# Kernel tuning notes

Hardware: AMD Instinct MI355X
Metric: run time of the kernel (lower is better)

## Reference

```python
import jax, jax.numpy as jnp
import numpy as np

ENERGY = 0.4  # target low-frequency energy ratio (ctor default energy=0.4)


def setup_inputs() -> dict:
    key = jax.random.key(0)
    x = jax.random.normal(key, (8, 64, 256, 256), dtype=jnp.float32)
    return {"x": x}


def _min_cutoff_map(H, W):
    """For each pixel of the fftshifted spectrum, the smallest cutoff c such that
    the pixel lies inside the central box [crow-c:crow+c, ccol-c:ccol+c].
    A pixel (r, cc) is inside iff c >= max(-dr, dr+1) and c >= max(-dc, dc+1)."""
    crow, ccol = H // 2, W // 2
    dr = np.arange(H) - crow
    dc = np.arange(W) - ccol
    mr = np.maximum(-dr, dr + 1)
    mc = np.maximum(-dc, dc + 1)
    return np.maximum(mr[:, None], mc[None, :]).astype(np.int32)  # [H, W]


def reference(x):
    B, C, H, W = x.shape
    # fp32 FFT (matches the autocast-disabled fft in the original)
    fshift = jnp.fft.fftshift(jnp.fft.fft2(x.astype(jnp.float32)), axes=(-2, -1))

    minc = jnp.asarray(_min_cutoff_map(H, W))          # [H, W] int32
    nseg = max(H // 2, W // 2) + 1                      # static
    K = min(H, W) // 2                                  # candidates are 1..K-1

    # Radial (box) cumulative energy profile of channel 0, one pass per sample.
    mag2 = jnp.abs(fshift[:, 0]) ** 2                   # [B, H, W]
    ids = minc.reshape(-1)
    per_box = jax.vmap(
        lambda m: jax.ops.segment_sum(m.reshape(-1), ids, num_segments=nseg)
    )(mag2)                                             # [B, nseg]
    cum = jnp.cumsum(per_box, axis=-1)                  # cum[b, c] = box-energy at cutoff c
    total = cum[:, -1]
    target = ENERGY * total

    found = cum[:, 1:K] >= target[:, None]              # candidates c = 1..K-1
    first = jnp.argmax(found, axis=-1) + 1              # smallest satisfying c
    cutoff = jnp.where(jnp.any(found, axis=-1), first, 5)  # fallback 5, as in torch

    # Zero the central box per sample (broadcast over channels), then inverse FFT.
    keep = (minc[None, None, :, :] > cutoff[:, None, None, None]).astype(jnp.float32)
    hp = fshift * keep
    out = jnp.abs(jnp.fft.ifft2(jnp.fft.ifftshift(hp, axes=(-2, -1))))
    return out
```

## Files before the change

### kernel.cpp

```cpp
#include <hip/hip_runtime.h>
#include <hip/hip_fp16.h>
#include <math.h>

#define RESERVE 16384

__device__ __forceinline__ float2 cadd(float2 a, float2 b){ return make_float2(a.x+b.x, a.y+b.y); }
__device__ __forceinline__ float2 csub(float2 a, float2 b){ return make_float2(a.x-b.x, a.y-b.y); }
__device__ __forceinline__ float2 cmul(float2 a, float2 b){ return make_float2(a.x*b.x - a.y*b.y, a.x*b.y + a.y*b.x); }
__device__ __forceinline__ float2 cmulc(float2 a, float2 b){
  return make_float2(a.x*b.x + a.y*b.y, a.x*b.y - a.y*b.x); }
__device__ __forceinline__ __half2 f2h(float2 v){ return __floats2half2_rn(v.x, v.y); }
__device__ __forceinline__ float2 h2f(__half2 h){ return __half22float2(h); }

#define SCHED_FENCE() __builtin_amdgcn_sched_barrier(0x7F)

__device__ __forceinline__ constexpr int rho4(int r) { return ((r & 3) << 2) | (r >> 2); }

template<int DIR> __device__ __forceinline__ float2 twc(float2 z, float c, float s) {
  const float si = (DIR < 0) ? s : -s;
  return make_float2(c*z.x - si*z.y, c*z.y + si*z.x);
}
template<int DIR> __device__ __forceinline__ float2 mulmi(float2 z) {
  return (DIR < 0) ? make_float2(z.y, -z.x) : make_float2(-z.y, z.x);
}

template<int DIR, bool REV>
__device__ __forceinline__ void fft16(float2* v) {
  #define IX(i) (REV ? rho4(i) : (i))
  #pragma unroll
  for (int j0 = 0; j0 < 4; ++j0) {
    float2 a0 = v[IX(j0)], a1 = v[IX(j0+4)], a2 = v[IX(j0+8)], a3 = v[IX(j0+12)];
    float2 t0 = cadd(a0,a2), t1 = csub(a0,a2), t2 = cadd(a1,a3), d = csub(a1,a3);
    float2 t3 = (DIR < 0) ? make_float2(d.y,-d.x) : make_float2(-d.y,d.x);
    v[IX(j0)]    = cadd(t0,t2);
    v[IX(j0+4)]  = cadd(t1,t3);
    v[IX(j0+8)]  = csub(t0,t2);
    v[IX(j0+12)] = csub(t1,t3);
  }
  v[IX(5)]  = twc<DIR>(v[IX(5)],  0.92387953f, -0.38268343f);
  v[IX(6)]  = twc<DIR>(v[IX(6)],  0.70710678f, -0.70710678f);
  v[IX(7)]  = twc<DIR>(v[IX(7)],  0.38268343f, -0.92387953f);
  v[IX(9)]  = twc<DIR>(v[IX(9)],  0.70710678f, -0.70710678f);
  v[IX(10)] = mulmi<DIR>(v[IX(10)]);
  v[IX(11)] = twc<DIR>(v[IX(11)], -0.70710678f, -0.70710678f);
  v[IX(13)] = twc<DIR>(v[IX(13)],  0.38268343f, -0.92387953f);
  v[IX(14)] = twc<DIR>(v[IX(14)], -0.70710678f, -0.70710678f);
  v[IX(15)] = twc<DIR>(v[IX(15)], -0.92387953f,  0.38268343f);
  #pragma unroll
  for (int k1 = 0; k1 < 4; ++k1) {
    float2 a0 = v[IX(4*k1)], a1 = v[IX(4*k1+1)], a2 = v[IX(4*k1+2)], a3 = v[IX(4*k1+3)];
    float2 t0 = cadd(a0,a2), t1 = csub(a0,a2), t2 = cadd(a1,a3), d = csub(a1,a3);
    float2 t3 = (DIR < 0) ? make_float2(d.y,-d.x) : make_float2(-d.y,d.x);
    v[IX(4*k1)]   = cadd(t0,t2);
    v[IX(4*k1+1)] = cadd(t1,t3);
    v[IX(4*k1+2)] = csub(t0,t2);
    v[IX(4*k1+3)] = csub(t1,t3);
  }
  #undef IX
}

__device__ __forceinline__ void make_twf(int l, float2* twf) {
  float s, c;
  sincospif((float)l * (-1.0f/128.0f), &s, &c);
  const float2 w = make_float2(c, s);
  twf[0] = make_float2(1.f, 0.f);
  #pragma unroll
  for (int k = 1; k < 16; ++k) twf[k] = cmul(twf[k-1], w);
}

template<int DIR, bool REV1, bool HB>
__device__ __forceinline__ void fft256g(float2* v, void* trb, int l, const float2* twf) {
  fft16<DIR, REV1>(v);
  if (HB) {
    __half2* t = (__half2*)trb;
    #pragma unroll
    for (int r = 0; r < 16; ++r) {
      const int k1 = REV1 ? r : rho4(r);
      float2 z = v[r];
      z = (DIR < 0) ? cmul(twf[k1], z) : cmulc(twf[k1], z);
      t[k1 * 17 + l] = f2h(z);
    }
    SCHED_FENCE();
    #pragma unroll
    for (int j = 0; j < 16; ++j) v[j] = h2f(t[l * 17 + j]);
  } else {
    float2* t = (float2*)trb;
    #pragma unroll
    for (int r = 0; r < 16; ++r) {
      const int k1 = REV1 ? r : rho4(r);
      float2 z = v[r];
      z = (DIR < 0) ? cmul(twf[k1], z) : cmulc(twf[k1], z);
      t[k1 * 17 + l] = z;
    }
    SCHED_FENCE();
    #pragma unroll
    for (int j = 0; j < 16; ++j) v[j] = ((float2*)trb)[l * 17 + j];
  }
  SCHED_FENCE();
  fft16<DIR, false>(v);
}

#define GS32 276
#define GS16 280

__device__ __forceinline__ int SW(int row, int col) {
  return (row << 8) + (col ^ ((row & 7) << 2) ^ ((row & 1) << 4));
}
__device__ __forceinline__ int SW16(int r, int ul) {
  return (r << 4) + (ul ^ (r & 14));
}


__global__ __launch_bounds__(256) void k_pass1(const float* __restrict__ x,
    __half2* __restrict__ Bt, int img0, int istep) {
  __shared__ __align__(16) char smraw[16384];
  __shared__ __align__(16) float2 trbf[16 * GS32];
  float*   rowstage = (float*)smraw;
  __half2* outtile  = (__half2*)smraw;
  const int tid = threadIdx.x, g = tid >> 4, l = tid & 15;
  const int slot = blockIdx.y, img = img0 + slot * istep;
  const int r0 = blockIdx.x << 4;
  float2 twf[16]; make_twf(l, twf);
  const float* xsrc = x + ((size_t)img << 16) + (r0 << 8);
  #pragma unroll
  for (int it = 0; it < 4; ++it) {
    const int L = it * 1024 + tid * 4;
    const float4 d = *reinterpret_cast<const float4*>(xsrc + L);
    *reinterpret_cast<float4*>(rowstage + SW(L >> 8, L & 255)) = d;
  }
  __syncthreads();
  float2 v[16];
  #pragma unroll
  for (int j = 0; j < 16; ++j)
    v[j] = make_float2(rowstage[SW(g, l + (j << 4))], 0.f);
  __syncthreads();
  fft256g<-1, false, false>(v, trbf + g * GS32, l, twf);
  #pragma unroll
  for (int rr = 0; rr < 16; ++rr)
    outtile[SW(g, l + (rho4(rr) << 4))] = f2h(v[rr]);
  __syncthreads();
  __half2* bdst = Bt + ((size_t)slot << 16) + (r0 << 4);
  #pragma unroll
  for (int it = 0; it < 4; ++it) {
    const int L = it * 1024 + tid * 4;
    const int p = L >> 8, rl = (L >> 4) & 15, ul0 = L & 15;
    const int4 d = *reinterpret_cast<const int4*>(outtile + SW(rl, (p << 4) + ul0));
    *reinterpret_cast<int4*>(bdst + (p << 12) + (L & 255)) = d;
  }
}

__global__ __launch_bounds__(256) void k_pass2(const __half2* __restrict__ Bt,
    __half2* __restrict__ Ct, const int* __restrict__ cutoffs, int img0, int istep) {
  __shared__ __align__(16) char smraw[16384];
  __shared__ __align__(16) __half2 trbh[16 * GS16];
  __half2* instage = (__half2*)smraw;
  __half2* outtile = (__half2*)smraw;
  const int tid = threadIdx.x, g = tid >> 4, l = tid & 15;
  const int slot = blockIdx.y, img = img0 + slot * istep;
  const int p = blockIdx.x;
  const int cut = cutoffs[img >> 6];
  const __half2* bsrc = Bt + ((size_t)slot << 16) + (p << 12);
  __half2* cdst = Ct + ((size_t)slot << 16) + (p << 12);
  const bool kept = (p * 16 >= cut) && (p * 16 + 15 < 256 - cut);
  if (kept) {
    const __half2 s = __floats2half2_rn(256.f, 256.f);
    #pragma unroll
    for (int it = 0; it < 4; ++it) {
      const int L = it * 1024 + tid * 4;
      int4 d = *reinterpret_cast<const int4*>(bsrc + L);
      __half2* h = reinterpret_cast<__half2*>(&d);
      h[0] = __hmul2(h[0], s); h[1] = __hmul2(h[1], s);
      h[2] = __hmul2(h[2], s); h[3] = __hmul2(h[3], s);
      *reinterpret_cast<int4*>(cdst + L) = d;
    }
    return;
  }
  float2 twf[16]; make_twf(l, twf);
  #pragma unroll
  for (int it = 0; it < 4; ++it) {
    const int L = it * 1024 + tid * 4;
    const int4 d = *reinterpret_cast<const int4*>(bsrc + L);
    const int r = L >> 4, ul0 = L & 15;
    const int i0 = SW16(r, ul0);
    *reinterpret_cast<int2*>(instage + i0) = make_int2(d.x, d.y);
    *reinterpret_cast<int2*>(instage + (i0 ^ 2)) = make_int2(d.z, d.w);
  }
  __syncthreads();
  __half2 hv[16];
  #pragma unroll
  for (int j = 0; j < 16; ++j) hv[j] = instage[SW16(l + (j << 4), g)];
  __syncthreads();
  const int u = (p << 4) + g;
  float2 v[16];
  #pragma unroll
  for (int j = 0; j < 16; ++j) v[j] = h2f(hv[j]);
  fft256g<-1, false, true>(v, trbh + g * GS16, l, twf);
  if ((u < cut) | (u >= 256 - cut)) {
    #pragma unroll
    for (int rr = 0; rr < 16; ++rr) {
      const int vi = l + (rho4(rr) << 4);
      if (vi < cut || vi >= 256 - cut) v[rr] = make_float2(0.f, 0.f);
    }
  }
  fft256g<1, true, true>(v, trbh + g * GS16, l, twf);
  #pragma unroll
  for (int rr = 0; rr < 16; ++rr)
    outtile[SW16(l + (rho4(rr) << 4), g)] = f2h(v[rr]);
  __syncthreads();
  #pragma unroll
  for (int it = 0; it < 4; ++it) {
    const int L = it * 1024 + tid * 4;
    const int r = L >> 4, ul0 = L & 15;
    const int i0 = SW16(r, ul0);
    const int2 a = *reinterpret_cast<const int2*>(outtile + i0);
    const int2 b = *reinterpret_cast<const int2*>(outtile + (i0 ^ 2));
    *reinterpret_cast<int4*>(cdst + L) = make_int4(a.x, a.y, b.x, b.y);
  }
}

__global__ __launch_bounds__(256) void k_pass3(const __half2* __restrict__ Ct,
    float* __restrict__ out, int img0, int istep) {
  __shared__ __align__(16) char smraw[16384];
  __shared__ __align__(16) __half2 trbh[16 * GS16];
  __half2* instage  = (__half2*)smraw;
  float*   outstage = (float*)smraw;
  const int tid = threadIdx.x, g = tid >> 4, l = tid & 15;
  const int slot = blockIdx.y, img = img0 + slot * istep;
  const int r0 = blockIdx.x << 4;
  float2 twf[16]; make_twf(l, twf);
  #pragma unroll
  for (int k = 0; k < 16; ++k) { twf[k].x *= 0.0625f; twf[k].y *= 0.0625f; }
  const __half2* csrc = Ct + ((size_t)slot << 16) + (r0 << 4);
  #pragma unroll
  for (int it = 0; it < 4; ++it) {
    const int L = it * 1024 + tid * 4;
    const int p = L >> 8, rl = (L >> 4) & 15, ul0 = L & 15;
    const int4 d = *reinterpret_cast<const int4*>(csrc + (p << 12) + (L & 255));
    *reinterpret_cast<int4*>(instage + SW(rl, (p << 4) + ul0)) = d;
  }
  __syncthreads();
  __half2 hv[16];
  #pragma unroll
  for (int j = 0; j < 16; ++j) hv[j] = instage[SW(g, l + (j << 4))];
  __syncthreads();
  float2 v[16];
  #pragma unroll
  for (int j = 0; j < 16; ++j) v[j] = h2f(hv[j]);
  fft256g<1, false, true>(v, trbh + g * GS16, l, twf);
  #pragma unroll
  for (int rr = 0; rr < 16; ++rr) {
    const float2 z = v[rr];
    outstage[SW(g, l + (rho4(rr) << 4))] =
        __builtin_amdgcn_sqrtf(z.x*z.x + z.y*z.y) * (1.f/4096.f);
  }
  __syncthreads();
  float* odst = out + ((size_t)img << 16) + (r0 << 8);
  #pragma unroll
  for (int it = 0; it < 4; ++it) {
    const int L = it * 1024 + tid * 4;
    const float4 d = *reinterpret_cast<const float4*>(outstage + SW(L >> 8, L & 255));
    *reinterpret_cast<float4*>(odst + L) = d;
  }
}

__global__ __launch_bounds__(256) void k_hist(const __half2* __restrict__ Bt,
    double* __restrict__ bins, int slot0, int sstep, int batch0) {
  __shared__ __align__(16) __half2 instage[4096];
  __shared__ __align__(16) float2 trbf[16 * GS32];
  __shared__ float whist[4][132];
  const int tid = threadIdx.x, g = tid >> 4, l = tid & 15, wave = tid >> 6;
  const int lb = blockIdx.y;
  const int batch = batch0 + lb;
  const size_t slot = (size_t)(slot0 + lb * sstep);
  const int p = blockIdx.x;
  const int u = (p << 4) + g;
  float2 twf[16]; make_twf(l, twf);
  for (int i = tid & 63; i < 132; i += 64) whist[wave][i] = 0.f;
  const __half2* bsrc = Bt + (slot << 16) + (p << 12);
  #pragma unroll
  for (int it = 0; it < 4; ++it) {
    const int L = it * 1024 + tid * 4;
    const int4 d = *reinterpret_cast<const int4*>(bsrc + L);
    const int r = L >> 4, ul0 = L & 15;
    const int i0 = SW16(r, ul0);
    *reinterpret_cast<int2*>(instage + i0) = make_int2(d.x, d.y);
    *reinterpret_cast<int2*>(instage + (i0 ^ 2)) = make_int2(d.z, d.w);
  }
  __syncthreads();
  float2 v[16];
  #pragma unroll
  for (int j = 0; j < 16; ++j) v[j] = h2f(instage[SW16(l + (j << 4), g)]);
  fft256g<-1, false, false>(v, trbf + g * GS32, l, twf);
  const int fc = (u < 128) ? u + 1 : 256 - u;
  #pragma unroll
  for (int rr = 0; rr < 16; ++rr) {
    const int vi = l + (rho4(rr) << 4);
    const int fu = (vi < 128) ? vi + 1 : 256 - vi;
    const int seg = fu > fc ? fu : fc;
    const float2 z = v[rr];
    atomicAdd(&whist[wave][seg], z.x*z.x + z.y*z.y);
  }
  __syncthreads();
  for (int s = tid; s < 129; s += 256) {
    const float sum = whist[0][s] + whist[1][s] + whist[2][s] + whist[3][s];
    if (sum != 0.f) atomicAdd(&bins[batch * 129 + s], (double)sum);
  }
}

__global__ void k_cutoff(const double* __restrict__ bins, int* __restrict__ cutoffs) {
  const int b = threadIdx.x;
  if (b < 8) {
    const double* Bv = bins + b * 129;
    double total = 0.0;
    for (int s = 0; s < 129; ++s) total += Bv[s];
    const double target = 0.4 * total;
    double cum = Bv[0];
    int cut = 5;
    bool found = false;
    for (int s = 1; s <= 127; ++s) {
      cum += Bv[s];
      if (!found && cum >= target) { cut = s; found = true; }
    }
    cutoffs[b] = cut;
  }
}

extern "C" void kernel_launch(void* const* d_in, const int* in_sizes, int n_in,
                              void* d_out, int out_size, void* d_ws, size_t ws_size,
                              hipStream_t stream) {
  const float* x = (const float*)d_in[0];
  float* out = (float*)d_out;
  char* wsb = (char*)d_ws;
  double* bins    = (double*)wsb;
  int*    cutoffs = (int*)(wsb + 8448);
  char*   payload = wsb + RESERVE;

  size_t avail = (ws_size > RESERVE) ? ws_size - (size_t)RESERVE : 0;
  long long Gl = (long long)(avail / 524288);
  int G = (Gl > 512) ? 512 : (int)Gl;
  if (G < 1) G = 1;
  __half2* Bt = (__half2*)payload;
  __half2* Ct = (__half2*)(payload + (size_t)G * 262144);

  hipMemsetAsync(bins, 0, 8 * 129 * sizeof(double), stream);
  dim3 blk(256, 1, 1);

  if (G >= 512) {
    k_pass1<<<dim3(16, 512), blk, 0, stream>>>(x, Bt, 0, 1);
    k_hist <<<dim3(16, 8),   blk, 0, stream>>>(Bt, bins, 0, 64, 0);
    k_cutoff<<<dim3(1), dim3(64), 0, stream>>>(bins, cutoffs);
    k_pass2<<<dim3(16, 512), blk, 0, stream>>>(Bt, Ct, cutoffs, 0, 1);
    k_pass3<<<dim3(16, 512), blk, 0, stream>>>(Ct, out, 0, 1);
  } else {
    int Gp = G > 8 ? 8 : G;
    for (int b0 = 0; b0 < 8; b0 += Gp) {
      int n = (8 - b0 < Gp) ? (8 - b0) : Gp;
      k_pass1<<<dim3(16, n), blk, 0, stream>>>(x, Bt, b0 * 64, 64);
      k_hist <<<dim3(16, n), blk, 0, stream>>>(Bt, bins, 0, 1, b0);
    }
    k_cutoff<<<dim3(1), dim3(64), 0, stream>>>(bins, cutoffs);
    for (int g0 = 0; g0 < 512; g0 += G) {
      int n = (512 - g0 < G) ? (512 - g0) : G;
      k_pass1<<<dim3(16, n), blk, 0, stream>>>(x, Bt, g0, 1);
      k_pass2<<<dim3(16, n), blk, 0, stream>>>(Bt, Ct, cutoffs, g0, 1);
      k_pass3<<<dim3(16, n), blk, 0, stream>>>(Ct, out, g0, 1);
    }
  }
}
```

Measured before the change: 207.8 us.

## Exploit real-input Hermitian symmetry and alias shared-memory staging buffers

Pass1 now writes only column panels 0..8 of the row-FFT output for non-channel-0 images, since the input is real and the remaining columns are conjugates. Pass2 rebuilds the upper column panels by reading the mirrored column and negating its imaginary part. The separate transpose scratch buffers are merged into the staging buffer to cut LDS per block, which needs extra barriers. In exchange it adds strided uncoalesced column gathers in pass2, and channel 0 still writes all panels for the histogram.

Measured after the change: 216.8 us. +4.3%, slower.

```diff
diff --git a/kernel.cpp b/kernel.cpp
--- a/kernel.cpp
+++ b/kernel.cpp
@@ -113,13 +113,14 @@
 
 __global__ __launch_bounds__(256) void k_pass1(const float* __restrict__ x,
     __half2* __restrict__ Bt, int img0, int istep) {
-  __shared__ __align__(16) char smraw[16384];
-  __shared__ __align__(16) float2 trbf[16 * GS32];
+  __shared__ __align__(16) char smraw[16 * GS32 * 8];
   float*   rowstage = (float*)smraw;
   __half2* outtile  = (__half2*)smraw;
+  float2*  trbf     = (float2*)smraw;
   const int tid = threadIdx.x, g = tid >> 4, l = tid & 15;
   const int slot = blockIdx.y, img = img0 + slot * istep;
   const int r0 = blockIdx.x << 4;
+  const bool full = ((img & 63) == 0);
   float2 twf[16]; make_twf(l, twf);
   const float* xsrc = x + ((size_t)img << 16) + (r0 << 8);
   #pragma unroll
@@ -135,6 +136,7 @@
     v[j] = make_float2(rowstage[SW(g, l + (j << 4))], 0.f);
   __syncthreads();
   fft256g<-1, false, false>(v, trbf + g * GS32, l, twf);
+  __syncthreads();
   #pragma unroll
   for (int rr = 0; rr < 16; ++rr)
     outtile[SW(g, l + (rho4(rr) << 4))] = f2h(v[rr]);
@@ -144,58 +146,88 @@
   for (int it = 0; it < 4; ++it) {
     const int L = it * 1024 + tid * 4;
     const int p = L >> 8, rl = (L >> 4) & 15, ul0 = L & 15;
-    const int4 d = *reinterpret_cast<const int4*>(outtile + SW(rl, (p << 4) + ul0));
-    *reinterpret_cast<int4*>(bdst + (p << 12) + (L & 255)) = d;
+    if (p <= 8 || full) {
+      const int4 d = *reinterpret_cast<const int4*>(outtile + SW(rl, (p << 4) + ul0));
+      *reinterpret_cast<int4*>(bdst + (p << 12) + (L & 255)) = d;
+    }
   }
 }
 
 __global__ __launch_bounds__(256) void k_pass2(const __half2* __restrict__ Bt,
     __half2* __restrict__ Ct, const int* __restrict__ cutoffs, int img0, int istep) {
-  __shared__ __align__(16) char smraw[16384];
-  __shared__ __align__(16) __half2 trbh[16 * GS16];
+  __shared__ __align__(16) char smraw[16 * GS16 * 4];
   __half2* instage = (__half2*)smraw;
   __half2* outtile = (__half2*)smraw;
+  __half2* trbh    = (__half2*)smraw;
   const int tid = threadIdx.x, g = tid >> 4, l = tid & 15;
   const int slot = blockIdx.y, img = img0 + slot * istep;
   const int p = blockIdx.x;
   const int cut = cutoffs[img >> 6];
-  const __half2* bsrc = Bt + ((size_t)slot << 16) + (p << 12);
+  const int cc = (p << 4) + g;
+  const __half2* bimg = Bt + ((size_t)slot << 16);
   __half2* cdst = Ct + ((size_t)slot << 16) + (p << 12);
   const bool kept = (p * 16 >= cut) && (p * 16 + 15 < 256 - cut);
-  if (kept) {
-    const __half2 s = __floats2half2_rn(256.f, 256.f);
+  float2 twf[16]; make_twf(l, twf);
+  float2 v[16];
+  if (p < 8) {
+    const __half2* bsrc = bimg + (p << 12);
+    if (kept) {
+      const __half2 s = __floats2half2_rn(256.f, 256.f);
+      #pragma unroll
+      for (int it = 0; it < 4; ++it) {
+        const int L = it * 1024 + tid * 4;
+        int4 d = *reinterpret_cast<const int4*>(bsrc + L);
+        __half2* h = reinterpret_cast<__half2*>(&d);
+        h[0] = __hmul2(h[0], s); h[1] = __hmul2(h[1], s);
+        h[2] = __hmul2(h[2], s); h[3] = __hmul2(h[3], s);
+        *reinterpret_cast<int4*>(cdst + L) = d;
+      }
+      return;
+    }
     #pragma unroll
     for (int it = 0; it < 4; ++it) {
       const int L = it * 1024 + tid * 4;
-      int4 d = *reinterpret_cast<const int4*>(bsrc + L);
-      __half2* h = reinterpret_cast<__half2*>(&d);
-      h[0] = __hmul2(h[0], s); h[1] = __hmul2(h[1], s);
-      h[2] = __hmul2(h[2], s); h[3] = __hmul2(h[3], s);
-      *reinterpret_cast<int4*>(cdst + L) = d;
-    }
-    return;
-  }
-  float2 twf[16]; make_twf(l, twf);
-  #pragma unroll
-  for (int it = 0; it < 4; ++it) {
-    const int L = it * 1024 + tid * 4;
-    const int4 d = *reinterpret_cast<const int4*>(bsrc + L);
-    const int r = L >> 4, ul0 = L & 15;
-    const int i0 = SW16(r, ul0);
-    *reinterpret_cast<int2*>(instage + i0) = make_int2(d.x, d.y);
-    *reinterpret_cast<int2*>(instage + (i0 ^ 2)) = make_int2(d.z, d.w);
-  }
-  __syncthreads();
-  __half2 hv[16];
-  #pragma unroll
-  for (int j = 0; j < 16; ++j) hv[j] = instage[SW16(l + (j << 4), g)];
-  __syncthreads();
-  const int u = (p << 4) + g;
-  float2 v[16];
-  #pragma unroll
-  for (int j = 0; j < 16; ++j) v[j] = h2f(hv[j]);
+      const int4 d = *reinterpret_cast<const int4*>(bsrc + L);
+      const int r = L >> 4, ul0 = L & 15;
+      const int i0 = SW16(r, ul0);
+      *reinterpret_cast<int2*>(instage + i0) = make_int2(d.x, d.y);
+      *reinterpret_cast<int2*>(instage + (i0 ^ 2)) = make_int2(d.z, d.w);
+    }
+    __syncthreads();
+    __half2 hv[16];
+    #pragma unroll
+    for (int j = 0; j < 16; ++j) hv[j] = instage[SW16(l + (j << 4), g)];
+    __syncthreads();
+    #pragma unroll
+    for (int j = 0; j < 16; ++j) v[j] = h2f(hv[j]);
+  } else {
+    int u; float csign;
+    if (cc <= 128) { u = cc; csign = 1.f; } else { u = 256 - cc; csign = -1.f; }
+    const __half2* colsrc = bimg + ((u >> 4) << 12) + (u & 15);
+    #pragma unroll
+    for (int j = 0; j < 16; ++j) {
+      float2 z = h2f(colsrc[(l + (j << 4)) << 4]);
+      v[j] = make_float2(z.x, z.y * csign);
+    }
+    if (kept) {
+      #pragma unroll
+      for (int j = 0; j < 16; ++j)
+        outtile[SW16(l + (j << 4), g)] = f2h(make_float2(v[j].x * 256.f, v[j].y * 256.f));
+      __syncthreads();
+      #pragma unroll
+      for (int it = 0; it < 4; ++it) {
+        const int L = it * 1024 + tid * 4;
+        const int r = L >> 4, ul0 = L & 15;
+        const int i0 = SW16(r, ul0);
+        const int2 a = *reinterpret_cast<const int2*>(outtile + i0);
+        const int2 b = *reinterpret_cast<const int2*>(outtile + (i0 ^ 2));
+        *reinterpret_cast<int4*>(cdst + L) = make_int4(a.x, a.y, b.x, b.y);
+      }
+      return;
+    }
+  }
   fft256g<-1, false, true>(v, trbh + g * GS16, l, twf);
-  if ((u < cut) | (u >= 256 - cut)) {
+  if ((cc < cut) | (cc >= 256 - cut)) {
     #pragma unroll
     for (int rr = 0; rr < 16; ++rr) {
       const int vi = l + (rho4(rr) << 4);
@@ -203,6 +235,7 @@
     }
   }
   fft256g<1, true, true>(v, trbh + g * GS16, l, twf);
+  __syncthreads();
   #pragma unroll
   for (int rr = 0; rr < 16; ++rr)
     outtile[SW16(l + (rho4(rr) << 4), g)] = f2h(v[rr]);
@@ -220,10 +253,10 @@
 
 __global__ __launch_bounds__(256) void k_pass3(const __half2* __restrict__ Ct,
     float* __restrict__ out, int img0, int istep) {
-  __shared__ __align__(16) char smraw[16384];
-  __shared__ __align__(16) __half2 trbh[16 * GS16];
+  __shared__ __align__(16) char smraw[16 * GS16 * 4];
   __half2* instage  = (__half2*)smraw;
   float*   outstage = (float*)smraw;
+  __half2* trbh     = (__half2*)smraw;
   const int tid = threadIdx.x, g = tid >> 4, l = tid & 15;
   const int slot = blockIdx.y, img = img0 + slot * istep;
   const int r0 = blockIdx.x << 4;
@@ -247,6 +280,7 @@
   #pragma unroll
   for (int j = 0; j < 16; ++j) v[j] = h2f(hv[j]);
   fft256g<1, false, true>(v, trbh + g * GS16, l, twf);
+  __syncthreads();
   #pragma unroll
   for (int rr = 0; rr < 16; ++rr) {
     const float2 z = v[rr];
```
